# Performance work log

Hardware: AMD Instinct MI355X
Metric: run time of the kernel (lower is better)

Reference implementation:

```python
import jax, jax.numpy as jnp
import numpy as np

VN, BN, NSW, EC, MN = 64, 200, 10, 63, 73
FIN, HID = 32, 64
VLOW, VUPP = 0.9, 1.1


def _ln(z, eps=1e-5):
    m = jnp.mean(z, axis=-1, keepdims=True)
    v = jnp.var(z, axis=-1, keepdims=True)
    return (z - m) * jax.lax.rsqrt(v + eps)


def _layer(x, s, conn, deg_inv, Ws, Wi, Wj, U, Vw, first):
    # dense gated edge update over (B,V,V,H)
    e = jnp.einsum('bvwh,hk->bvwk', s, Ws) + (x @ Wi)[:, :, None, :] + (x @ Wj)[:, None, :, :]
    e = jax.nn.relu(_ln(e))
    s_out = e if first else s + e
    gate = jax.nn.sigmoid(s_out) * conn[None, :, :, None]
    msg = jnp.einsum('bvwh,bwh->bvh', gate, x @ Vw) * deg_inv[None, :, None]  # mean agg
    h = jax.nn.relu(_ln(x @ U + msg))
    return (h if first else x + h), s_out


def setup_inputs() -> dict:
    key = jax.random.key(0)
    ks = jax.random.split(key, 24)
    # radial feeder: path graph (line edges) + long-range tie switches, i<j (triu)
    ea = np.stack([np.arange(VN - 1), np.arange(1, VN)]).astype(np.int32)
    es = np.stack([np.arange(NSW), np.arange(NSW) + 32]).astype(np.int32)
    A = np.zeros((VN, VN), np.float32); A[ea[0], ea[1]] = 1; A[ea[1], ea[0]] = 1
    S = np.zeros((VN, VN), np.float32); S[es[0], es[1]] = 1; S[es[1], es[0]] = 1
    par = np.concatenate([ea[0], es[0]]); chi = np.concatenate([ea[1], es[1]])
    Incp = np.zeros((VN, MN), np.float32); Incp[par, np.arange(MN)] = 1
    Incc = np.zeros((VN, MN), np.float32); Incc[chi, np.arange(MN)] = 1
    deg = (A + S).sum(1)
    Dinv = np.diag((1.0 / np.maximum(deg, 1.0)).astype(np.float32))

    def w(k, shape):
        return jax.random.normal(k, shape, jnp.float32) / np.sqrt(shape[-2])

    return {
        'x': jax.random.normal(ks[0], (BN, VN, FIN), jnp.float32),
        'A': jnp.asarray(A), 'S': jnp.asarray(S),
        'embed_s': jax.random.normal(ks[1], (2, FIN), jnp.float32),
        'p0_Ws': w(ks[2], (FIN, HID)), 'p0_Wi': w(ks[3], (FIN, HID)),
        'p0_Wj': w(ks[4], (FIN, HID)), 'p0_U': w(ks[5], (FIN, HID)),
        'p0_V': w(ks[6], (FIN, HID)),
        'pl_Ws': w(ks[7], (2, HID, HID)), 'pl_Wi': w(ks[8], (2, HID, HID)),
        'pl_Wj': w(ks[9], (2, HID, HID)), 'pl_U': w(ks[10], (2, HID, HID)),
        'pl_V': w(ks[11], (2, HID, HID)),
        'smlp_W1': w(ks[12], (4 * HID, 4 * HID)), 'smlp_W2': w(ks[13], (4 * HID, 4)),
        'cmlp_W1': w(ks[14], (3 * HID, 3 * HID)), 'cmlp_W2': w(ks[15], (3 * HID, 3)),
        'Dinv': jnp.asarray(Dinv), 'Incp': jnp.asarray(Incp), 'Incc': jnp.asarray(Incc),
        'edge_A': jnp.asarray(ea), 'edge_S': jnp.asarray(es),
    }


def reference(x, A, S, embed_s, p0_Ws, p0_Wi, p0_Wj, p0_U, p0_V,
              pl_Ws, pl_Wi, pl_Wj, pl_U, pl_V,
              smlp_W1, smlp_W2, cmlp_W1, cmlp_W2,
              Dinv, Incp, Incc, edge_A, edge_S):
    B = x.shape[0]
    conn = jnp.clip(A + S, 0.0, 1.0)                       # (V,V) union adjacency
    deg_inv = 1.0 / jnp.maximum(conn.sum(1), 1.0)
    # init_embed_edges over dense S -> (B,V,V,FIN)
    s = jnp.broadcast_to(embed_s[S.astype(jnp.int32)][None], (B, VN, VN, FIN))
    xh, s = _layer(x, s, conn, deg_inv, p0_Ws, p0_Wi, p0_Wj, p0_U, p0_V, True)
    for l in range(pl_Ws.shape[0]):
        xh, s = _layer(xh, s, conn, deg_inv, pl_Ws[l], pl_Wi[l], pl_Wj[l], pl_U[l], pl_V[l], False)
    x_g = xh.sum(1)                                        # (B,H) graph feature

    # -- switch head (gather at triu switch edges, identical across batch) --
    si, sj = edge_S[0], edge_S[1]
    xg_s = jnp.broadcast_to(x_g[:, None, :], (B, si.shape[0], HID))
    smlp_in = jnp.concatenate([s[:, si, sj, :], xh[:, si], xh[:, sj], xg_s], axis=-1)
    smlp_out = jax.nn.sigmoid(jax.nn.relu(smlp_in @ smlp_W1) @ smlp_W2)  # (B,nsw,4)
    topology = smlp_out[..., 0]
    graph_topo = jnp.concatenate([jnp.ones((B, MN - NSW), x.dtype), topology], axis=1)
    ps = smlp_out[..., 1] - 0.5
    vs_p = VLOW * (1 - smlp_out[..., 2]) + VUPP * smlp_out[..., 2]
    vs_c = VLOW * (1 - smlp_out[..., 3]) + VUPP * smlp_out[..., 3]

    # -- connection head (gather at triu line edges) --
    ai, aj = edge_A[0], edge_A[1]
    xg_c = jnp.broadcast_to(x_g[:, None, :], (B, ai.shape[0], HID))
    cmlp_in = jnp.concatenate([xh[:, ai], xh[:, aj], xg_c], axis=-1)
    cmlp_out = jax.nn.sigmoid(jax.nn.relu(cmlp_in @ cmlp_W1) @ cmlp_W2)  # (B,Ec,3)
    pc = cmlp_out[..., 0] - 0.5
    vc_p = VLOW * (1 - cmlp_out[..., 1]) + VUPP * cmlp_out[..., 1]
    vc_c = VLOW * (1 - cmlp_out[..., 2]) + VUPP * cmlp_out[..., 2]

    # scatter into (B,M) physics tensors: first M-nsw cols from CMLP, last nsw from SMLP
    p_flow = jnp.concatenate([pc, ps], axis=1)
    v_par = jnp.concatenate([vc_p, vs_p], axis=1)
    v_chi = jnp.concatenate([vc_c, vs_c], axis=1)
    v = v_par @ (Dinv @ Incp).T + v_chi @ (Dinv @ Incc).T   # (B,V)
    v = v.at[:, 0].set(1.0)
    return jnp.concatenate([p_flow, v, graph_topo], axis=1)  # (B, M+V+M)
```

## Files before the change

### kernel.cpp

```cpp
#include <hip/hip_runtime.h>

#define BN 200
#define VN 64
#define HIDD 64
#define FINN 32
#define NSW 10
#define EC 63
#define MNE 73
#define NEDGE 146
#define NPACK 128

typedef unsigned short u16;
typedef unsigned int u32;
typedef __attribute__((ext_vector_type(8))) short bf16x8;
typedef __attribute__((ext_vector_type(4))) float f32x4;

__device__ __forceinline__ float bfu(u16 u) { return __uint_as_float(((u32)u) << 16); }
__device__ __forceinline__ u16 f2bf(float f) {
    u32 x = __float_as_uint(f);
    u32 r = x + 0x7fffu + ((x >> 16) & 1u);
    return (u16)(r >> 16);
}
__device__ __forceinline__ float cvtv(const void* p, int i, int fl) {
    return fl ? bfu(((const u16*)p)[i]) : ((const float*)p)[i];
}

__device__ __forceinline__ int swz(int row, int col) { return col ^ ((row & 7) << 3); }

__device__ __forceinline__ float ldp(const u16* H, const u16* L, int idx) {
    return bfu(H[idx]) + bfu(L[idx]);
}
__device__ __forceinline__ void stp(u16* H, u16* L, int idx, float f) {
    u16 h = f2bf(f);
    H[idx] = h;
    L[idx] = f2bf(f - bfu(h));
}

__device__ __forceinline__ float ln_relu64(float e) {
    float s1 = e, s2 = e * e;
#pragma unroll
    for (int m = 1; m < 64; m <<= 1) {
        s1 += __shfl_xor(s1, m);
        s2 += __shfl_xor(s2, m);
    }
    float mean = s1 * 0.015625f;
    float var = fmaxf(s2 * 0.015625f - mean * mean, 0.f);
    return fmaxf((e - mean) * rsqrtf(var + 1e-5f), 0.f);
}

struct CvtArgs { const void* src[21]; };

__global__ __launch_bounds__(256) void k_prep(CvtArgs ca, const int* __restrict__ eA,
                                              const int* __restrict__ eS,
                                              u16* __restrict__ c1h, u16* __restrict__ c1l,
                                              u16* __restrict__ c2h, u16* __restrict__ c2l,
                                              u16* __restrict__ s1h, u16* __restrict__ s1l,
                                              u16* __restrict__ s2h, u16* __restrict__ s2l,
                                              u16* __restrict__ w0h, u16* __restrict__ w0l,
                                              u16* __restrict__ wlh, u16* __restrict__ wll,
                                              float* __restrict__ ews, float* __restrict__ dinv,
                                              int* __restrict__ row_ptr, int* __restrict__ colp,
                                              int* __restrict__ sw_eidx,
                                              float* __restrict__ dinvD, int* __restrict__ incCnt,
                                              int* __restrict__ incM) {
    int t = threadIdx.x;
    int fl = (((const u16*)ca.src[1])[1] == 0x3F80) ? 1 : 0;
    if (blockIdx.x == 0) {
        __shared__ unsigned char flagL[64 * 65];
        __shared__ float wsL[FINN * 64];
        __shared__ float emL[64];
        __shared__ int degL[64], rpS[65], colS[NEDGE + 16];
        __shared__ int eAL[2 * EC], eSL[2 * NSW];

        if (t < 2 * EC) eAL[t] = eA[t];
        if (t >= 128 && t < 128 + 2 * NSW) eSL[t - 128] = eS[t - 128];
        if (t >= 160 && t < 224) emL[t - 160] = cvtv(ca.src[3], t - 160, fl);
        for (int i = t; i < FINN * 64; i += 256) wsL[i] = cvtv(ca.src[4], i, fl);
        for (int i = t; i < 4096; i += 256) {
            float a = cvtv(ca.src[1], i, fl);
            float s = cvtv(ca.src[2], i, fl);
            int r = i >> 6, c = i & 63;
            flagL[r * 65 + c] = (unsigned char)(((a != 0.f || s != 0.f) ? 1 : 0) |
                                                ((s != 0.f) ? 2 : 0));
        }
        __syncthreads();

        if (t < 128) {
            int j = t >> 6, k = t & 63;
            float a = 0.f;
#pragma unroll
            for (int h = 0; h < FINN; h++) a += emL[j * FINN + h] * wsL[h * 64 + k];
            ews[(j << 6) + k] = a;
        }
        if (t < 64) {
            int d = 0;
#pragma unroll
            for (int w = 0; w < 64; w++) d += flagL[t * 65 + w] & 1;
            degL[t] = d;
            dinv[t] = 1.f / fmaxf((float)d, 1.f);
        }
        __syncthreads();
        if (t == 0) {
            int c = 0;
            for (int v = 0; v < 64; v++) { rpS[v] = c; c += degL[v]; }
            rpS[64] = c;
        }
        __syncthreads();
        if (t < 65) row_ptr[t] = rpS[t];
        if (t < 64) {
            int pos = rpS[t];
#pragma unroll
            for (int w = 0; w < 64; w++) {
                int f = flagL[t * 65 + w];
                if (f & 1) colS[pos++] = w | ((f & 2) ? 256 : 0);
            }
        }
        __syncthreads();
        int tot = rpS[64];
        if (t < tot) colp[t] = colS[t];
        if (t < NSW) {
            int si = eSL[t], sj = eSL[NSW + t];
            int idx = 0;
            for (int e = rpS[si]; e < rpS[si + 1]; e++)
                if ((colS[e] & 255) == sj) idx = e;
            sw_eidx[t] = idx;
        }
        if (t < 64) {
            dinvD[t] = cvtv(ca.src[18], t * 64 + t, fl);
            int cnt = 0;
            for (int m = 0; m < MNE; m++) {
                int par = (m < EC) ? eAL[m] : eSL[m - EC];
                int chi = (m < EC) ? eAL[EC + m] : eSL[NSW + (m - EC)];
                if (par == t && cnt < 8) incM[t * 8 + cnt++] = (m << 1);
                if (chi == t && cnt < 8) incM[t * 8 + cnt++] = (m << 1) | 1;
            }
            incCnt[t] = cnt;
        }
    } else {
        const int T1 = 36864, T2 = T1 + 3072, T3 = T2 + 65536, T4 = T3 + 4096;
        const int T5 = T4 + 8192, TOT = T5 + 40960;
        for (int i = (blockIdx.x - 1) * 256 + t; i < TOT; i += NPACK * 256) {
            int idx = i;
            const void* src;
            u16 *dh, *dl;
            int K2, N2, nt, rem, loff = 0;
            if (idx < T1) {
                nt = idx / 3072; rem = idx - nt * 3072; src = ca.src[16];
                dh = c1h + idx; dl = c1l + idx; K2 = 192; N2 = 192;
            } else if (idx < T2) {
                idx -= T1; nt = 0; rem = idx; src = ca.src[17];
                dh = c2h + idx; dl = c2l + idx; K2 = 192; N2 = 3;
            } else if (idx < T3) {
                idx -= T2; nt = idx >> 12; rem = idx & 4095; src = ca.src[14];
                dh = s1h + idx; dl = s1l + idx; K2 = 256; N2 = 256;
            } else if (idx < T4) {
                idx -= T3; nt = 0; rem = idx; src = ca.src[15];
                dh = s2h + idx; dl = s2l + idx; K2 = 256; N2 = 4;
            } else if (idx < T5) {
                int j = idx - T4;
                int mt = j >> 11;
                int m2 = j & 2047;
                nt = m2 >> 9; rem = m2 & 511; src = ca.src[5 + mt];
                dh = w0h + j; dl = w0l + j; K2 = 32; N2 = 64;
            } else {
                int j = idx - T5;
                int l = j / 20480;
                int jj = j - l * 20480;
                int mt = jj >> 12;
                int m2 = jj & 4095;
                nt = m2 >> 10; rem = m2 & 1023; src = ca.src[9 + mt];
                loff = l * 4096;
                dh = wlh + j; dl = wll + j; K2 = 64; N2 = 64;
            }
            int kb = rem >> 9, r8 = rem & 511, ln = r8 >> 3, jq = r8 & 7;
            int k = kb * 32 + ((ln >> 4) << 3) + jq;
            int n = nt * 16 + (ln & 15);
            float val = 0.f;
            if (n < N2 && k < K2) val = cvtv(src, loff + k * N2 + n, fl);
            u16 h = f2bf(val);
            *dh = h;
            *dl = f2bf(val - bfu(h));
        }
    }
}

#define XI 0
#define XJ 1
#define XU 2
#define XV 3

__global__ __launch_bounds__(1024) void k_main(
    const void* __restrict__ xraw, const u16* __restrict__ A_u16,
    const int* __restrict__ eA, const int* __restrict__ eS,
    const float* __restrict__ ews, const float* __restrict__ dinv,
    const int* __restrict__ row_ptr, const int* __restrict__ colp,
    const int* __restrict__ sw_eidx,
    const float* __restrict__ dinvD, const int* __restrict__ incCnt, const int* __restrict__ incM,
    const u16* __restrict__ w0h, const u16* __restrict__ w0l,
    const u16* __restrict__ wlh, const u16* __restrict__ wll,
    const u16* __restrict__ c1h, const u16* __restrict__ c1l,
    const u16* __restrict__ c2h, const u16* __restrict__ c2l,
    const u16* __restrict__ s1h, const u16* __restrict__ s1l,
    const u16* __restrict__ s2h, const u16* __restrict__ s2l,
    void* __restrict__ out_v)
{
    __shared__ __align__(16) u16 xHp[64 * 64], xLp[64 * 64];
    __shared__ __align__(16) u16 sHp[NEDGE * 64], sLp[NEDGE * 64];
    __shared__ __align__(16) float preL[NEDGE * 64];
    __shared__ __align__(16) float tLs[4 * 64 * 64];
    __shared__ __align__(16) u16 xgH[64], xgLo[64];
    __shared__ float ewsL[128];
    __shared__ float dinvL[64];
    __shared__ int rpL[65];
    __shared__ int colL[NEDGE + 6];
    __shared__ int swLx[NSW];
    __shared__ float cmoL[EC * 3], smoL[NSW * 4];

    int b = blockIdx.x, t = threadIdx.x;
    int lane = t & 63, wid = t >> 6;
    int m = lane & 15, quad = lane >> 4;
    int fl = (A_u16[1] == 0x3F80) ? 1 : 0;

    for (int i = t; i < 2048; i += 1024) {
        int r = i >> 5, c = i & 31;
        stp(xHp, xLp, (r << 6) + swz(r, c), cvtv(xraw, b * 2048 + i, fl));
    }
    if (t < 128) ewsL[t] = ews[t];
    if (t < 64) dinvL[t] = dinv[t];
    if (t < 65) rpL[t] = row_ptr[t];
    if (t < NEDGE) colL[t] = colp[t];
    if (t < NSW) swLx[t] = sw_eidx[t];
    __syncthreads();

    {
        int mat = wid >> 2, Mt = wid & 3;
        const u16* bhp = w0h + mat * 2048;
        const u16* blp = w0l + mat * 2048;
        int row = Mt * 16 + m;
        int c0 = quad * 8;
        bf16x8 ah = *(const bf16x8*)&xHp[(row << 6) + swz(row, c0)];
        bf16x8 al = *(const bf16x8*)&xLp[(row << 6) + swz(row, c0)];
        f32x4 acc[4];
#pragma unroll
        for (int nt = 0; nt < 4; nt++) acc[nt] = (f32x4){0.f, 0.f, 0.f, 0.f};
#pragma unroll
        for (int nt = 0; nt < 4; nt++) {
            int o = (nt << 9) + (lane << 3);
            bf16x8 bh = *(const bf16x8*)(bhp + o);
            bf16x8 bl = *(const bf16x8*)(blp + o);
            acc[nt] = __builtin_amdgcn_mfma_f32_16x16x32_bf16(ah, bh, acc[nt], 0, 0, 0);
            acc[nt] = __builtin_amdgcn_mfma_f32_16x16x32_bf16(al, bh, acc[nt], 0, 0, 0);
            acc[nt] = __builtin_amdgcn_mfma_f32_16x16x32_bf16(ah, bl, acc[nt], 0, 0, 0);
        }
#pragma unroll
        for (int nt = 0; nt < 4; nt++)
#pragma unroll
            for (int r = 0; r < 4; r++) {
                int orow = Mt * 16 + quad * 4 + r;
                tLs[mat * 4096 + (orow << 6) + swz(orow, nt * 16 + m)] = acc[nt][r];
            }
    }
    __syncthreads();

    {
#pragma unroll
        for (int q = 0; q < 4; q++) {
            int v = (wid << 2) + q;
            int e0 = rpL[v], e1 = rpL[v + 1];
            float xival = tLs[XI * 4096 + (v << 6) + swz(v, lane)];
            float macc = 0.f;
            for (int e = e0; e < e1; e++) {
                int cp = colL[e];
                int w = cp & 255;
                float ee = ewsL[(((cp >> 8) & 1) << 6) + lane] + xival
                         + tLs[XJ * 4096 + (w << 6) + swz(w, lane)];
                float sout = ln_relu64(ee);
                stp(sHp, sLp, (e << 6) + swz(e, lane), sout);
                macc += tLs[XV * 4096 + (w << 6) + swz(w, lane)] / (1.f + __expf(-sout));
            }
            float z = tLs[XU * 4096 + (v << 6) + swz(v, lane)] + macc * dinvL[v];
            stp(xHp, xLp, (v << 6) + swz(v, lane), ln_relu64(z));
        }
    }
    __syncthreads();

    for (int l = 0; l < 2; l++) {
        {
            int mat = wid >> 2, Mt = wid & 3;
            const u16* bhp = wlh + l * 20480 + (mat + 1) * 4096;
            const u16* blp = wll + l * 20480 + (mat + 1) * 4096;
            int row = Mt * 16 + m;
            f32x4 acc[4];
#pragma unroll
            for (int nt = 0; nt < 4; nt++) acc[nt] = (f32x4){0.f, 0.f, 0.f, 0.f};
#pragma unroll
            for (int kb = 0; kb < 2; kb++) {
                int c0 = kb * 32 + quad * 8;
                bf16x8 ah = *(const bf16x8*)&xHp[(row << 6) + swz(row, c0)];
                bf16x8 al = *(const bf16x8*)&xLp[(row << 6) + swz(row, c0)];
#pragma unroll
                for (int nt = 0; nt < 4; nt++) {
                    int o = (((nt << 1) + kb) << 9) + (lane << 3);
                    bf16x8 bh = *(const bf16x8*)(bhp + o);
                    bf16x8 bl = *(const bf16x8*)(blp + o);
                    acc[nt] = __builtin_amdgcn_mfma_f32_16x16x32_bf16(ah, bh, acc[nt], 0, 0, 0);
                    acc[nt] = __builtin_amdgcn_mfma_f32_16x16x32_bf16(al, bh, acc[nt], 0, 0, 0);
                    acc[nt] = __builtin_amdgcn_mfma_f32_16x16x32_bf16(ah, bl, acc[nt], 0, 0, 0);
                }
            }
#pragma unroll
            for (int nt = 0; nt < 4; nt++)
#pragma unroll
                for (int r = 0; r < 4; r++) {
                    int orow = Mt * 16 + quad * 4 + r;
                    tLs[mat * 4096 + (orow << 6) + swz(orow, nt * 16 + m)] = acc[nt][r];
                }

            if (wid < 10) {
                const u16* sbh = wlh + l * 20480;
                const u16* sbl = wll + l * 20480;
                int srow = wid * 16 + m;
                int ar = (srow > NEDGE - 1) ? (NEDGE - 1) : srow;
                f32x4 sacc[4];
#pragma unroll
                for (int nt = 0; nt < 4; nt++) sacc[nt] = (f32x4){0.f, 0.f, 0.f, 0.f};
#pragma unroll
                for (int kb = 0; kb < 2; kb++) {
                    int c0 = kb * 32 + quad * 8;
                    bf16x8 ah = *(const bf16x8*)&sHp[(ar << 6) + swz(ar, c0)];
                    bf16x8 al = *(const bf16x8*)&sLp[(ar << 6) + swz(ar, c0)];
#pragma unroll
                    for (int nt = 0; nt < 4; nt++) {
                        int o = (((nt << 1) + kb) << 9) + (lane << 3);
                        bf16x8 bh = *(const bf16x8*)(sbh + o);
                        bf16x8 bl = *(const bf16x8*)(sbl + o);
                        sacc[nt] = __builtin_amdgcn_mfma_f32_16x16x32_bf16(ah, bh, sacc[nt], 0, 0, 0);
                        sacc[nt] = __builtin_amdgcn_mfma_f32_16x16x32_bf16(al, bh, sacc[nt], 0, 0, 0);
                        sacc[nt] = __builtin_amdgcn_mfma_f32_16x16x32_bf16(ah, bl, sacc[nt], 0, 0, 0);
                    }
                }
#pragma unroll
                for (int nt = 0; nt < 4; nt++)
#pragma unroll
                    for (int r = 0; r < 4; r++) {
                        int orow = wid * 16 + quad * 4 + r;
                        if (orow < NEDGE)
                            preL[(orow << 6) + swz(orow, nt * 16 + m)] = sacc[nt][r];
                    }
            }
        }
        __syncthreads();

        {
#pragma unroll
            for (int q = 0; q < 4; q++) {
                int v = (wid << 2) + q;
                int e0 = rpL[v], e1 = rpL[v + 1];
                float xival = tLs[XI * 4096 + (v << 6) + swz(v, lane)];
                float macc = 0.f;
                for (int e = e0; e < e1; e++) {
                    int cp = colL[e];
                    int w = cp & 255;
                    int sidx = (e << 6) + swz(e, lane);
                    float ee = preL[sidx] + xival
                             + tLs[XJ * 4096 + (w << 6) + swz(w, lane)];
                    float sout = ldp(sHp, sLp, sidx) + ln_relu64(ee);
                    stp(sHp, sLp, sidx, sout);
                    macc += tLs[XV * 4096 + (w << 6) + swz(w, lane)] / (1.f + __expf(-sout));
                }
                float z = tLs[XU * 4096 + (v << 6) + swz(v, lane)] + macc * dinvL[v];
                float h = ln_relu64(z);
                int xidx = (v << 6) + swz(v, lane);
                stp(xHp, xLp, xidx, ldp(xHp, xLp, xidx) + h);
            }
        }
        __syncthreads();
    }

    u16* tp  = (u16*)tLs;
    u16* hcH = tp;
    u16* hcL = tp + 12288;
    u16* hsH = tp + 24576;
    u16* hsL = tp + 28672;
    float* xgP = preL;

    {
        float a = 0.f;
#pragma unroll
        for (int q = 0; q < 4; q++) {
            int r = (wid << 2) + q;
            a += ldp(xHp, xLp, (r << 6) + swz(r, lane));
        }
        xgP[wid * 64 + lane] = a;
    }
    __syncthreads();
    if (t < 64) {
        float s = 0.f;
#pragma unroll
        for (int i = 0; i < 16; i++) s += xgP[i * 64 + t];
        stp(xgH, xgLo, t, s);
    }
    __syncthreads();

    {
        int Mt = wid >> 2, ntb = wid & 3;
        int e = Mt * 16 + m; if (e > 62) e = 62;
        int ai = eA[e], aj = eA[EC + e];
        f32x4 acc[3];
#pragma unroll
        for (int j3 = 0; j3 < 3; j3++) acc[j3] = (f32x4){0.f, 0.f, 0.f, 0.f};
#pragma unroll
        for (int kb = 0; kb < 6; kb++) {
            int k = kb * 32 + quad * 8;
            bf16x8 ah, al;
            if (k < 64) {
                ah = *(const bf16x8*)&xHp[(ai << 6) + swz(ai, k)];
                al = *(const bf16x8*)&xLp[(ai << 6) + swz(ai, k)];
            } else if (k < 128) {
                int c = k - 64;
                ah = *(const bf16x8*)&xHp[(aj << 6) + swz(aj, c)];
                al = *(const bf16x8*)&xLp[(aj << 6) + swz(aj, c)];
            } else {
                int c = k - 128;
                ah = *(const bf16x8*)&xgH[c];
                al = *(const bf16x8*)&xgLo[c];
            }
#pragma unroll
            for (int j3 = 0; j3 < 3; j3++) {
                int nt = ntb + j3 * 4;
                int o = ((nt * 6 + kb) << 9) + (lane << 3);
                bf16x8 bh = *(const bf16x8*)(c1h + o);
                bf16x8 bl = *(const bf16x8*)(c1l + o);
                acc[j3] = __builtin_amdgcn_mfma_f32_16x16x32_bf16(ah, bh, acc[j3], 0, 0, 0);
                acc[j3] = __builtin_amdgcn_mfma_f32_16x16x32_bf16(al, bh, acc[j3], 0, 0, 0);
                acc[j3] = __builtin_amdgcn_mfma_f32_16x16x32_bf16(ah, bl, acc[j3], 0, 0, 0);
            }
        }
        __syncthreads();
#pragma unroll
        for (int j3 = 0; j3 < 3; j3++) {
            int nt = ntb + j3 * 4;
#pragma unroll
            for (int r = 0; r < 4; r++) {
                int row = Mt * 16 + quad * 4 + r;
                stp(hcH, hcL, row * 192 + swz(row, nt * 16 + m), fmaxf(acc[j3][r], 0.f));
            }
        }
    }
    __syncthreads();

    if (wid < 4) {
        f32x4 accD = (f32x4){0.f, 0.f, 0.f, 0.f};
        int row = wid * 16 + m;
#pragma unroll
        for (int kb = 0; kb < 6; kb++) {
            int c0 = kb * 32 + quad * 8;
            bf16x8 ah = *(const bf16x8*)&hcH[row * 192 + swz(row, c0)];
            bf16x8 al = *(const bf16x8*)&hcL[row * 192 + swz(row, c0)];
            int o = (kb << 9) + (lane << 3);
            bf16x8 bh = *(const bf16x8*)(c2h + o);
            bf16x8 bl = *(const bf16x8*)(c2l + o);
            accD = __builtin_amdgcn_mfma_f32_16x16x32_bf16(ah, bh, accD, 0, 0, 0);
            accD = __builtin_amdgcn_mfma_f32_16x16x32_bf16(al, bh, accD, 0, 0, 0);
            accD = __builtin_amdgcn_mfma_f32_16x16x32_bf16(ah, bl, accD, 0, 0, 0);
        }
#pragma unroll
        for (int r = 0; r < 4; r++) {
            int row2 = wid * 16 + quad * 4 + r;
            if (row2 < EC && m < 3)
                cmoL[row2 * 3 + m] = 1.f / (1.f + __expf(-accD[r]));
        }
    }
    __syncthreads();

    {
        int e2 = (m > 9) ? 9 : m;
        int si = eS[e2], sj = eS[NSW + e2];
        int sw = swLx[e2];
        f32x4 accS = (f32x4){0.f, 0.f, 0.f, 0.f};
#pragma unroll
        for (int kb = 0; kb < 8; kb++) {
            int k = kb * 32 + quad * 8;
            bf16x8 ah, al;
            if (k < 64) {
                ah = *(const bf16x8*)&sHp[(sw << 6) + swz(sw, k)];
                al = *(const bf16x8*)&sLp[(sw << 6) + swz(sw, k)];
            } else if (k < 128) {
                int c = k - 64;
                ah = *(const bf16x8*)&xHp[(si << 6) + swz(si, c)];
                al = *(const bf16x8*)&xLp[(si << 6) + swz(si, c)];
            } else if (k < 192) {
                int c = k - 128;
                ah = *(const bf16x8*)&xHp[(sj << 6) + swz(sj, c)];
                al = *(const bf16x8*)&xLp[(sj << 6) + swz(sj, c)];
            } else {
                int c = k - 192;
                ah = *(const bf16x8*)&xgH[c];
                al = *(const bf16x8*)&xgLo[c];
            }
            int o = ((wid * 8 + kb) << 9) + (lane << 3);
            bf16x8 bh = *(const bf16x8*)(s1h + o);
            bf16x8 bl = *(const bf16x8*)(s1l + o);
            accS = __builtin_amdgcn_mfma_f32_16x16x32_bf16(ah, bh, accS, 0, 0, 0);
            accS = __builtin_amdgcn_mfma_f32_16x16x32_bf16(al, bh, accS, 0, 0, 0);
            accS = __builtin_amdgcn_mfma_f32_16x16x32_bf16(ah, bl, accS, 0, 0, 0);
        }
#pragma unroll
        for (int r = 0; r < 4; r++) {
            int row = quad * 4 + r;
            stp(hsH, hsL, (row << 8) + swz(row, wid * 16 + m), fmaxf(accS[r], 0.f));
        }
    }
    __syncthreads();

    if (wid == 0) {
        f32x4 accT = (f32x4){0.f, 0.f, 0.f, 0.f};
#pragma unroll
        for (int kb = 0; kb < 8; kb++) {
            int c0 = kb * 32 + quad * 8;
            bf16x8 ah = *(const bf16x8*)&hsH[(m << 8) + swz(m, c0)];
            bf16x8 al = *(const bf16x8*)&hsL[(m << 8) + swz(m, c0)];
            int o = (kb << 9) + (lane << 3);
            bf16x8 bh = *(const bf16x8*)(s2h + o);
            bf16x8 bl = *(const bf16x8*)(s2l + o);
            accT = __builtin_amdgcn_mfma_f32_16x16x32_bf16(ah, bh, accT, 0, 0, 0);
            accT = __builtin_amdgcn_mfma_f32_16x16x32_bf16(al, bh, accT, 0, 0, 0);
            accT = __builtin_amdgcn_mfma_f32_16x16x32_bf16(ah, bl, accT, 0, 0, 0);
        }
#pragma unroll
        for (int r = 0; r < 4; r++) {
            int row = quad * 4 + r;
            if (row < NSW && m < 4)
                smoL[row * 4 + m] = 1.f / (1.f + __expf(-accT[r]));
        }
    }
    __syncthreads();

    if (t < 2 * MNE + VN) {
        float val;
        if (t < MNE) {
            val = (t < EC) ? cmoL[t * 3] - 0.5f : smoL[(t - EC) * 4 + 1] - 0.5f;
        } else if (t < MNE + VN) {
            int i = t - MNE;
            if (i == 0) {
                val = 1.0f;
            } else {
                float acc = 0.f;
                int c = incCnt[i];
                for (int q = 0; q < c; q++) {
                    int em = incM[i * 8 + q];
                    int mm = em >> 1, role = em & 1;
                    float vv = (mm < EC) ? 0.9f + 0.2f * cmoL[mm * 3 + 1 + role]
                                         : 0.9f + 0.2f * smoL[(mm - EC) * 4 + 2 + role];
                    acc += vv;
                }
                val = acc * dinvD[i];
            }
        } else {
            int mm = t - (MNE + VN);
            val = (mm < EC) ? 1.0f : smoL[(mm - EC) * 4];
        }
        size_t oidx = (size_t)b * (2 * MNE + VN) + t;
        if (fl) ((u16*)out_v)[oidx] = f2bf(val);
        else    ((float*)out_v)[oidx] = val;
    }
}

extern "C" void kernel_launch(void* const* d_in, const int* in_sizes, int n_in,
                              void* d_out, int out_size, void* d_ws, size_t ws_size,
                              hipStream_t stream) {
    const int* eA = (const int*)d_in[21];
    const int* eS = (const int*)d_in[22];

    float* pool = (float*)d_ws;
    float* ews     = pool;
    float* dinv    = ews + 128;
    float* dinvD   = dinv + 64;
    int*   row_ptr = (int*)(dinvD + 64);
    int*   colp    = row_ptr + 80;
    int*   sw_eidx = colp + 256;
    int*   incCnt  = sw_eidx + 16;
    int*   incM    = incCnt + 64;
    u16*   c1h = (u16*)(incM + 512);
    u16*   c1l = c1h + 36864;
    u16*   c2h = c1l + 36864;
    u16*   c2l = c2h + 3072;
    u16*   s1h = c2l + 3072;
    u16*   s1l = s1h + 65536;
    u16*   s2h = s1l + 65536;
    u16*   s2l = s2h + 4096;
    u16*   w0h = s2l + 4096;
    u16*   w0l = w0h + 8192;
    u16*   wlh = w0l + 8192;
    u16*   wll = wlh + 40960;

    CvtArgs ca;
    for (int i = 0; i < 21; i++) ca.src[i] = d_in[i];

    k_prep<<<1 + NPACK, 256, 0, stream>>>(ca, eA, eS,
                                          c1h, c1l, c2h, c2l, s1h, s1l, s2h, s2l,
                                          w0h, w0l, wlh, wll,
                                          ews, dinv, row_ptr, colp, sw_eidx,
                                          dinvD, incCnt, incM);

    k_main<<<BN, 1024, 0, stream>>>(d_in[0], (const u16*)d_in[1], eA, eS,
                                    ews, dinv, row_ptr, colp, sw_eidx,
                                    dinvD, incCnt, incM,
                                    w0h, w0l, wlh, wll,
                                    c1h, c1l, c2h, c2l, s1h, s1l, s2h, s2l,
                                    d_out);
}
```

Measured before the change: 177.1 us.

## Parallelize edge updates across waves, batch layernorm reductions, merge MLP head phases

Splits the per-node edge loop into an edge-parallel pass (two edges per wave, with the source node packed into the column index) that writes gated messages to shared memory, followed by a per-node aggregation with a four-way batched layernorm reduction. Redistributes the edge-state matmul across all 16 waves, computes the graph pooling sum during the last layer, and runs the connection and switch MLP first stages concurrently on different waves, removing barriers. Edge-index arrays are staged in shared memory. The cost is more shared-memory round trips through preL and some extra barriers per layer.

```diff
diff --git a/kernel.cpp b/kernel.cpp
--- a/kernel.cpp
+++ b/kernel.cpp
@@ -36,16 +36,43 @@
     L[idx] = f2bf(f - bfu(h));
 }
 
-__device__ __forceinline__ float ln_relu64(float e) {
-    float s1 = e, s2 = e * e;
+__device__ __forceinline__ void ln2(float ea, float eb, float& ra, float& rb) {
+    float a1 = ea, a2 = ea * ea, b1 = eb, b2 = eb * eb;
 #pragma unroll
     for (int m = 1; m < 64; m <<= 1) {
-        s1 += __shfl_xor(s1, m);
-        s2 += __shfl_xor(s2, m);
-    }
-    float mean = s1 * 0.015625f;
-    float var = fmaxf(s2 * 0.015625f - mean * mean, 0.f);
-    return fmaxf((e - mean) * rsqrtf(var + 1e-5f), 0.f);
+        a1 += __shfl_xor(a1, m);
+        a2 += __shfl_xor(a2, m);
+        b1 += __shfl_xor(b1, m);
+        b2 += __shfl_xor(b2, m);
+    }
+    float ma = a1 * 0.015625f, mb = b1 * 0.015625f;
+    float va = fmaxf(a2 * 0.015625f - ma * ma, 0.f);
+    float vb = fmaxf(b2 * 0.015625f - mb * mb, 0.f);
+    ra = fmaxf((ea - ma) * rsqrtf(va + 1e-5f), 0.f);
+    rb = fmaxf((eb - mb) * rsqrtf(vb + 1e-5f), 0.f);
+}
+
+__device__ __forceinline__ void ln4(float ea, float eb, float ec, float ed,
+                                    float& ra, float& rb, float& rc, float& rd) {
+    float a1 = ea, a2 = ea * ea, b1 = eb, b2 = eb * eb;
+    float c1 = ec, c2 = ec * ec, d1 = ed, d2 = ed * ed;
+#pragma unroll
+    for (int m = 1; m < 64; m <<= 1) {
+        a1 += __shfl_xor(a1, m); a2 += __shfl_xor(a2, m);
+        b1 += __shfl_xor(b1, m); b2 += __shfl_xor(b2, m);
+        c1 += __shfl_xor(c1, m); c2 += __shfl_xor(c2, m);
+        d1 += __shfl_xor(d1, m); d2 += __shfl_xor(d2, m);
+    }
+    float ma = a1 * 0.015625f, mb = b1 * 0.015625f;
+    float mc = c1 * 0.015625f, md = d1 * 0.015625f;
+    float va = fmaxf(a2 * 0.015625f - ma * ma, 0.f);
+    float vb = fmaxf(b2 * 0.015625f - mb * mb, 0.f);
+    float vc = fmaxf(c2 * 0.015625f - mc * mc, 0.f);
+    float vd = fmaxf(d2 * 0.015625f - md * md, 0.f);
+    ra = fmaxf((ea - ma) * rsqrtf(va + 1e-5f), 0.f);
+    rb = fmaxf((eb - mb) * rsqrtf(vb + 1e-5f), 0.f);
+    rc = fmaxf((ec - mc) * rsqrtf(vc + 1e-5f), 0.f);
+    rd = fmaxf((ed - md) * rsqrtf(vd + 1e-5f), 0.f);
 }
 
 struct CvtArgs { const void* src[21]; };
@@ -112,7 +139,7 @@
 #pragma unroll
             for (int w = 0; w < 64; w++) {
                 int f = flagL[t * 65 + w];
-                if (f & 1) colS[pos++] = w | ((f & 2) ? 256 : 0);
+                if (f & 1) colS[pos++] = w | ((f & 2) ? 256 : 0) | (t << 16);
             }
         }
         __syncthreads();
@@ -214,6 +241,7 @@
     __shared__ int rpL[65];
     __shared__ int colL[NEDGE + 6];
     __shared__ int swLx[NSW];
+    __shared__ int eALs[2 * EC], eSLs[2 * NSW];
     __shared__ float cmoL[EC * 3], smoL[NSW * 4];
 
     int b = blockIdx.x, t = threadIdx.x;
@@ -230,6 +258,8 @@
     if (t < 65) rpL[t] = row_ptr[t];
     if (t < NEDGE) colL[t] = colp[t];
     if (t < NSW) swLx[t] = sw_eidx[t];
+    if (t >= 256 && t < 256 + 2 * EC) eALs[t - 256] = eA[t - 256];
+    if (t >= 512 && t < 512 + 2 * NSW) eSLs[t - 512] = eS[t - 512];
     __syncthreads();
 
     {
@@ -262,25 +292,51 @@
     }
     __syncthreads();
 
+    for (int e = wid; e < NEDGE; e += 32) {
+        int e2i = e + 16;
+        int has2 = (e2i < NEDGE);
+        int eb2 = has2 ? e2i : e;
+        int cpa = colL[e], cpb = colL[eb2];
+        int wa = cpa & 255, va = (cpa >> 16) & 255;
+        int wb = cpb & 255, vb = (cpb >> 16) & 255;
+        int sia = (e << 6) + swz(e, lane);
+        int sib = (eb2 << 6) + swz(eb2, lane);
+        float eea = ewsL[(((cpa >> 8) & 1) << 6) + lane]
+                  + tLs[XI * 4096 + (va << 6) + swz(va, lane)]
+                  + tLs[XJ * 4096 + (wa << 6) + swz(wa, lane)];
+        float eeb = ewsL[(((cpb >> 8) & 1) << 6) + lane]
+                  + tLs[XI * 4096 + (vb << 6) + swz(vb, lane)]
+                  + tLs[XJ * 4096 + (wb << 6) + swz(wb, lane)];
+        float ha, hb;
+        ln2(eea, eeb, ha, hb);
+        stp(sHp, sLp, sia, ha);
+        preL[sia] = tLs[XV * 4096 + (wa << 6) + swz(wa, lane)]
+                  * __fdividef(1.f, 1.f + __expf(-ha));
+        if (has2) {
+            stp(sHp, sLp, sib, hb);
+            preL[sib] = tLs[XV * 4096 + (wb << 6) + swz(wb, lane)]
+                      * __fdividef(1.f, 1.f + __expf(-hb));
+        }
+    }
+    __syncthreads();
+
     {
-#pragma unroll
-        for (int q = 0; q < 4; q++) {
-            int v = (wid << 2) + q;
-            int e0 = rpL[v], e1 = rpL[v + 1];
-            float xival = tLs[XI * 4096 + (v << 6) + swz(v, lane)];
-            float macc = 0.f;
-            for (int e = e0; e < e1; e++) {
-                int cp = colL[e];
-                int w = cp & 255;
-                float ee = ewsL[(((cp >> 8) & 1) << 6) + lane] + xival
-                         + tLs[XJ * 4096 + (w << 6) + swz(w, lane)];
-                float sout = ln_relu64(ee);
-                stp(sHp, sLp, (e << 6) + swz(e, lane), sout);
-                macc += tLs[XV * 4096 + (w << 6) + swz(w, lane)] / (1.f + __expf(-sout));
-            }
-            float z = tLs[XU * 4096 + (v << 6) + swz(v, lane)] + macc * dinvL[v];
-            stp(xHp, xLp, (v << 6) + swz(v, lane), ln_relu64(z));
-        }
+        int v0 = wid << 2;
+        float mc0 = 0.f, mc1 = 0.f, mc2 = 0.f, mc3 = 0.f;
+        for (int e = rpL[v0]; e < rpL[v0 + 1]; e++) mc0 += preL[(e << 6) + swz(e, lane)];
+        for (int e = rpL[v0 + 1]; e < rpL[v0 + 2]; e++) mc1 += preL[(e << 6) + swz(e, lane)];
+        for (int e = rpL[v0 + 2]; e < rpL[v0 + 3]; e++) mc2 += preL[(e << 6) + swz(e, lane)];
+        for (int e = rpL[v0 + 3]; e < rpL[v0 + 4]; e++) mc3 += preL[(e << 6) + swz(e, lane)];
+        float z0 = tLs[XU * 4096 + ((v0 + 0) << 6) + swz(v0 + 0, lane)] + mc0 * dinvL[v0 + 0];
+        float z1 = tLs[XU * 4096 + ((v0 + 1) << 6) + swz(v0 + 1, lane)] + mc1 * dinvL[v0 + 1];
+        float z2 = tLs[XU * 4096 + ((v0 + 2) << 6) + swz(v0 + 2, lane)] + mc2 * dinvL[v0 + 2];
+        float z3 = tLs[XU * 4096 + ((v0 + 3) << 6) + swz(v0 + 3, lane)] + mc3 * dinvL[v0 + 3];
+        float h0, h1, h2, h3;
+        ln4(z0, z1, z2, z3, h0, h1, h2, h3);
+        stp(xHp, xLp, ((v0 + 0) << 6) + swz(v0 + 0, lane), h0);
+        stp(xHp, xLp, ((v0 + 1) << 6) + swz(v0 + 1, lane), h1);
+        stp(xHp, xLp, ((v0 + 2) << 6) + swz(v0 + 2, lane), h2);
+        stp(xHp, xLp, ((v0 + 3) << 6) + swz(v0 + 3, lane), h3);
     }
     __syncthreads();
 
@@ -316,99 +372,116 @@
                     tLs[mat * 4096 + (orow << 6) + swz(orow, nt * 16 + m)] = acc[nt][r];
                 }
 
-            if (wid < 10) {
-                const u16* sbh = wlh + l * 20480;
-                const u16* sbl = wll + l * 20480;
-                int srow = wid * 16 + m;
+            const u16* sbh = wlh + l * 20480;
+            const u16* sbl = wll + l * 20480;
+            for (int u = wid; u < 40; u += 16) {
+                int rt = u >> 2, ntq = u & 3;
+                int srow = rt * 16 + m;
                 int ar = (srow > NEDGE - 1) ? (NEDGE - 1) : srow;
-                f32x4 sacc[4];
-#pragma unroll
-                for (int nt = 0; nt < 4; nt++) sacc[nt] = (f32x4){0.f, 0.f, 0.f, 0.f};
+                f32x4 sacc = (f32x4){0.f, 0.f, 0.f, 0.f};
 #pragma unroll
                 for (int kb = 0; kb < 2; kb++) {
                     int c0 = kb * 32 + quad * 8;
                     bf16x8 ah = *(const bf16x8*)&sHp[(ar << 6) + swz(ar, c0)];
                     bf16x8 al = *(const bf16x8*)&sLp[(ar << 6) + swz(ar, c0)];
-#pragma unroll
-                    for (int nt = 0; nt < 4; nt++) {
-                        int o = (((nt << 1) + kb) << 9) + (lane << 3);
-                        bf16x8 bh = *(const bf16x8*)(sbh + o);
-                        bf16x8 bl = *(const bf16x8*)(sbl + o);
-                        sacc[nt] = __builtin_amdgcn_mfma_f32_16x16x32_bf16(ah, bh, sacc[nt], 0, 0, 0);
-                        sacc[nt] = __builtin_amdgcn_mfma_f32_16x16x32_bf16(al, bh, sacc[nt], 0, 0, 0);
-                        sacc[nt] = __builtin_amdgcn_mfma_f32_16x16x32_bf16(ah, bl, sacc[nt], 0, 0, 0);
-                    }
+                    int o = (((ntq << 1) + kb) << 9) + (lane << 3);
+                    bf16x8 bh = *(const bf16x8*)(sbh + o);
+                    bf16x8 bl = *(const bf16x8*)(sbl + o);
+                    sacc = __builtin_amdgcn_mfma_f32_16x16x32_bf16(ah, bh, sacc, 0, 0, 0);
+                    sacc = __builtin_amdgcn_mfma_f32_16x16x32_bf16(al, bh, sacc, 0, 0, 0);
+                    sacc = __builtin_amdgcn_mfma_f32_16x16x32_bf16(ah, bl, sacc, 0, 0, 0);
                 }
 #pragma unroll
-                for (int nt = 0; nt < 4; nt++)
-#pragma unroll
-                    for (int r = 0; r < 4; r++) {
-                        int orow = wid * 16 + quad * 4 + r;
-                        if (orow < NEDGE)
-                            preL[(orow << 6) + swz(orow, nt * 16 + m)] = sacc[nt][r];
-                    }
+                for (int r = 0; r < 4; r++) {
+                    int orow = rt * 16 + quad * 4 + r;
+                    if (orow < NEDGE)
+                        preL[(orow << 6) + swz(orow, ntq * 16 + m)] = sacc[r];
+                }
             }
         }
         __syncthreads();
 
+        for (int e = wid; e < NEDGE; e += 32) {
+            int e2i = e + 16;
+            int has2 = (e2i < NEDGE);
+            int eb2 = has2 ? e2i : e;
+            int cpa = colL[e], cpb = colL[eb2];
+            int wa = cpa & 255, va = (cpa >> 16) & 255;
+            int wb = cpb & 255, vb = (cpb >> 16) & 255;
+            int sia = (e << 6) + swz(e, lane);
+            int sib = (eb2 << 6) + swz(eb2, lane);
+            float eea = preL[sia]
+                      + tLs[XI * 4096 + (va << 6) + swz(va, lane)]
+                      + tLs[XJ * 4096 + (wa << 6) + swz(wa, lane)];
+            float eeb = preL[sib]
+                      + tLs[XI * 4096 + (vb << 6) + swz(vb, lane)]
+                      + tLs[XJ * 4096 + (wb << 6) + swz(wb, lane)];
+            float ha, hb;
+            ln2(eea, eeb, ha, hb);
+            float souta = ldp(sHp, sLp, sia) + ha;
+            float soutb = ldp(sHp, sLp, sib) + hb;
+            stp(sHp, sLp, sia, souta);
+            preL[sia] = tLs[XV * 4096 + (wa << 6) + swz(wa, lane)]
+                      * __fdividef(1.f, 1.f + __expf(-souta));
+            if (has2) {
+                stp(sHp, sLp, sib, soutb);
+                preL[sib] = tLs[XV * 4096 + (wb << 6) + swz(wb, lane)]
+                          * __fdividef(1.f, 1.f + __expf(-soutb));
+            }
+        }
+        __syncthreads();
+
         {
-#pragma unroll
-            for (int q = 0; q < 4; q++) {
-                int v = (wid << 2) + q;
-                int e0 = rpL[v], e1 = rpL[v + 1];
-                float xival = tLs[XI * 4096 + (v << 6) + swz(v, lane)];
-                float macc = 0.f;
-                for (int e = e0; e < e1; e++) {
-                    int cp = colL[e];
-                    int w = cp & 255;
-                    int sidx = (e << 6) + swz(e, lane);
-                    float ee = preL[sidx] + xival
-                             + tLs[XJ * 4096 + (w << 6) + swz(w, lane)];
-                    float sout = ldp(sHp, sLp, sidx) + ln_relu64(ee);
-                    stp(sHp, sLp, sidx, sout);
-                    macc += tLs[XV * 4096 + (w << 6) + swz(w, lane)] / (1.f + __expf(-sout));
-                }
-                float z = tLs[XU * 4096 + (v << 6) + swz(v, lane)] + macc * dinvL[v];
-                float h = ln_relu64(z);
-                int xidx = (v << 6) + swz(v, lane);
-                stp(xHp, xLp, xidx, ldp(xHp, xLp, xidx) + h);
-            }
+            int v0 = wid << 2;
+            float mc0 = 0.f, mc1 = 0.f, mc2 = 0.f, mc3 = 0.f;
+            for (int e = rpL[v0]; e < rpL[v0 + 1]; e++) mc0 += preL[(e << 6) + swz(e, lane)];
+            for (int e = rpL[v0 + 1]; e < rpL[v0 + 2]; e++) mc1 += preL[(e << 6) + swz(e, lane)];
+            for (int e = rpL[v0 + 2]; e < rpL[v0 + 3]; e++) mc2 += preL[(e << 6) + swz(e, lane)];
+            for (int e = rpL[v0 + 3]; e < rpL[v0 + 4]; e++) mc3 += preL[(e << 6) + swz(e, lane)];
+            float z0 = tLs[XU * 4096 + ((v0 + 0) << 6) + swz(v0 + 0, lane)] + mc0 * dinvL[v0 + 0];
+            float z1 = tLs[XU * 4096 + ((v0 + 1) << 6) + swz(v0 + 1, lane)] + mc1 * dinvL[v0 + 1];
+            float z2 = tLs[XU * 4096 + ((v0 + 2) << 6) + swz(v0 + 2, lane)] + mc2 * dinvL[v0 + 2];
+            float z3 = tLs[XU * 4096 + ((v0 + 3) << 6) + swz(v0 + 3, lane)] + mc3 * dinvL[v0 + 3];
+            float h0, h1, h2, h3;
+            ln4(z0, z1, z2, z3, h0, h1, h2, h3);
+            int i0 = ((v0 + 0) << 6) + swz(v0 + 0, lane);
+            int i1 = ((v0 + 1) << 6) + swz(v0 + 1, lane);
+            int i2 = ((v0 + 2) << 6) + swz(v0 + 2, lane);
+            int i3 = ((v0 + 3) << 6) + swz(v0 + 3, lane);
+            float x0 = ldp(xHp, xLp, i0) + h0;
+            float x1 = ldp(xHp, xLp, i1) + h1;
+            float x2 = ldp(xHp, xLp, i2) + h2;
+            float x3 = ldp(xHp, xLp, i3) + h3;
+            stp(xHp, xLp, i0, x0);
+            stp(xHp, xLp, i1, x1);
+            stp(xHp, xLp, i2, x2);
+            stp(xHp, xLp, i3, x3);
+            if (l == 1) tLs[(wid << 6) + lane] = x0 + x1 + x2 + x3;
         }
         __syncthreads();
     }
+
+    if (t < 64) {
+        float s = 0.f;
+#pragma unroll
+        for (int i = 0; i < 16; i++) s += tLs[(i << 6) + t];
+        stp(xgH, xgLo, t, s);
+    }
+    __syncthreads();
 
     u16* tp  = (u16*)tLs;
     u16* hcH = tp;
     u16* hcL = tp + 12288;
     u16* hsH = tp + 24576;
     u16* hsL = tp + 28672;
-    float* xgP = preL;
-
-    {
-        float a = 0.f;
-#pragma unroll
-        for (int q = 0; q < 4; q++) {
-            int r = (wid << 2) + q;
-            a += ldp(xHp, xLp, (r << 6) + swz(r, lane));
-        }
-        xgP[wid * 64 + lane] = a;
-    }
-    __syncthreads();
-    if (t < 64) {
-        float s = 0.f;
-#pragma unroll
-        for (int i = 0; i < 16; i++) s += xgP[i * 64 + t];
-        stp(xgH, xgLo, t, s);
-    }
-    __syncthreads();
-
-    {
-        int Mt = wid >> 2, ntb = wid & 3;
+
+    if (wid < 12) {
+        int Mt = wid & 3, ntg = wid >> 2;
         int e = Mt * 16 + m; if (e > 62) e = 62;
-        int ai = eA[e], aj = eA[EC + e];
-        f32x4 acc[3];
-#pragma unroll
-        for (int j3 = 0; j3 < 3; j3++) acc[j3] = (f32x4){0.f, 0.f, 0.f, 0.f};
+        int ai = eALs[e], aj = eALs[EC + e];
+        f32x4 acc[4];
+#pragma unroll
+        for (int j = 0; j < 4; j++) acc[j] = (f32x4){0.f, 0.f, 0.f, 0.f};
 #pragma unroll
         for (int kb = 0; kb < 6; kb++) {
             int k = kb * 32 + quad * 8;
@@ -426,24 +499,64 @@
                 al = *(const bf16x8*)&xgLo[c];
             }
 #pragma unroll
-            for (int j3 = 0; j3 < 3; j3++) {
-                int nt = ntb + j3 * 4;
+            for (int j = 0; j < 4; j++) {
+                int nt = ntg * 4 + j;
                 int o = ((nt * 6 + kb) << 9) + (lane << 3);
                 bf16x8 bh = *(const bf16x8*)(c1h + o);
                 bf16x8 bl = *(const bf16x8*)(c1l + o);
-                acc[j3] = __builtin_amdgcn_mfma_f32_16x16x32_bf16(ah, bh, acc[j3], 0, 0, 0);
-                acc[j3] = __builtin_amdgcn_mfma_f32_16x16x32_bf16(al, bh, acc[j3], 0, 0, 0);
-                acc[j3] = __builtin_amdgcn_mfma_f32_16x16x32_bf16(ah, bl, acc[j3], 0, 0, 0);
-            }
-        }
-        __syncthreads();
-#pragma unroll
-        for (int j3 = 0; j3 < 3; j3++) {
-            int nt = ntb + j3 * 4;
+                acc[j] = __builtin_amdgcn_mfma_f32_16x16x32_bf16(ah, bh, acc[j], 0, 0, 0);
+                acc[j] = __builtin_amdgcn_mfma_f32_16x16x32_bf16(al, bh, acc[j], 0, 0, 0);
+                acc[j] = __builtin_amdgcn_mfma_f32_16x16x32_bf16(ah, bl, acc[j], 0, 0, 0);
+            }
+        }
+#pragma unroll
+        for (int j = 0; j < 4; j++) {
+            int nt = ntg * 4 + j;
 #pragma unroll
             for (int r = 0; r < 4; r++) {
                 int row = Mt * 16 + quad * 4 + r;
-                stp(hcH, hcL, row * 192 + swz(row, nt * 16 + m), fmaxf(acc[j3][r], 0.f));
+                stp(hcH, hcL, row * 192 + swz(row, nt * 16 + m), fmaxf(acc[j][r], 0.f));
+            }
+        }
+    } else {
+        int e2 = (m > 9) ? 9 : m;
+        int si = eSLs[e2], sj = eSLs[NSW + e2];
+        int sw = swLx[e2];
+#pragma unroll
+        for (int j = 0; j < 4; j++) {
+            int nt = (wid - 12) * 4 + j;
+            f32x4 accS = (f32x4){0.f, 0.f, 0.f, 0.f};
+#pragma unroll
+            for (int kb = 0; kb < 8; kb++) {
+                int k = kb * 32 + quad * 8;
+                bf16x8 ah, al;
+                if (k < 64) {
+                    ah = *(const bf16x8*)&sHp[(sw << 6) + swz(sw, k)];
+                    al = *(const bf16x8*)&sLp[(sw << 6) + swz(sw, k)];
+                } else if (k < 128) {
+                    int c = k - 64;
+                    ah = *(const bf16x8*)&xHp[(si << 6) + swz(si, c)];
+                    al = *(const bf16x8*)&xLp[(si << 6) + swz(si, c)];
+                } else if (k < 192) {
+                    int c = k - 128;
+                    ah = *(const bf16x8*)&xHp[(sj << 6) + swz(sj, c)];
+                    al = *(const bf16x8*)&xLp[(sj << 6) + swz(sj, c)];
+                } else {
+                    int c = k - 192;
+                    ah = *(const bf16x8*)&xgH[c];
+                    al = *(const bf16x8*)&xgLo[c];
+                }
+                int o = ((nt * 8 + kb) << 9) + (lane << 3);
+                bf16x8 bh = *(const bf16x8*)(s1h + o);
+                bf16x8 bl = *(const bf16x8*)(s1l + o);
+                accS = __builtin_amdgcn_mfma_f32_16x16x32_bf16(ah, bh, accS, 0, 0, 0);
+                accS = __builtin_amdgcn_mfma_f32_16x16x32_bf16(al, bh, accS, 0, 0, 0);
+                accS = __builtin_amdgcn_mfma_f32_16x16x32_bf16(ah, bl, accS, 0, 0, 0);
+            }
+#pragma unroll
+            for (int r = 0; r < 4; r++) {
+                int row = quad * 4 + r;
+                stp(hsH, hsL, (row << 8) + swz(row, nt * 16 + m), fmaxf(accS[r], 0.f));
             }
         }
     }
@@ -470,50 +583,7 @@
             if (row2 < EC && m < 3)
                 cmoL[row2 * 3 + m] = 1.f / (1.f + __expf(-accD[r]));
         }
-    }
-    __syncthreads();
-
-    {
-        int e2 = (m > 9) ? 9 : m;
-        int si = eS[e2], sj = eS[NSW + e2];
-        int sw = swLx[e2];
-        f32x4 accS = (f32x4){0.f, 0.f, 0.f, 0.f};
-#pragma unroll
-        for (int kb = 0; kb < 8; kb++) {
-            int k = kb * 32 + quad * 8;
-            bf16x8 ah, al;
-            if (k < 64) {
-                ah = *(const bf16x8*)&sHp[(sw << 6) + swz(sw, k)];
-                al = *(const bf16x8*)&sLp[(sw << 6) + swz(sw, k)];
-            } else if (k < 128) {
-                int c = k - 64;
-                ah = *(const bf16x8*)&xHp[(si << 6) + swz(si, c)];
-                al = *(const bf16x8*)&xLp[(si << 6) + swz(si, c)];
-            } else if (k < 192) {
-                int c = k - 128;
-                ah = *(const bf16x8*)&xHp[(sj << 6) + swz(sj, c)];
-                al = *(const bf16x8*)&xLp[(sj << 6) + swz(sj, c)];
-            } else {
-                int c = k - 192;
-                ah = *(const bf16x8*)&xgH[c];
-                al = *(const bf16x8*)&xgLo[c];
-            }
-            int o = ((wid * 8 + kb) << 9) + (lane << 3);
-            bf16x8 bh = *(const bf16x8*)(s1h + o);
-            bf16x8 bl = *(const bf16x8*)(s1l + o);
-            accS = __builtin_amdgcn_mfma_f32_16x16x32_bf16(ah, bh, accS, 0, 0, 0);
-            accS = __builtin_amdgcn_mfma_f32_16x16x32_bf16(al, bh, accS, 0, 0, 0);
-            accS = __builtin_amdgcn_mfma_f32_16x16x32_bf16(ah, bl, accS, 0, 0, 0);
-        }
-#pragma unroll
-        for (int r = 0; r < 4; r++) {
-            int row = quad * 4 + r;
-            stp(hsH, hsL, (row << 8) + swz(row, wid * 16 + m), fmaxf(accS[r], 0.f));
-        }
-    }
-    __syncthreads();
-
-    if (wid == 0) {
+    } else if (wid == 4) {
         f32x4 accT = (f32x4){0.f, 0.f, 0.f, 0.f};
 #pragma unroll
         for (int kb = 0; kb < 8; kb++) {
```

Measured after the change: 179.7 us. No clear change (+1.5%).
